# Performance work log

Hardware: AMD Instinct MI355X
Metric: run time of the kernel (lower is better)

Reference implementation:

```python
import jax, jax.numpy as jnp
import numpy as np

B, L, J, CL, CJ, DM, NH, NB, OBS = 8192, 32, 31, 4, 8, 64, 4, 3, 128
TOK = CL * 16  # 64, flattened per-link token size
HD = DM // NH


def _ln(x, g, b):
    m = x.mean(-1, keepdims=True)
    v = ((x - m) ** 2).mean(-1, keepdims=True)
    return (x - m) / jnp.sqrt(v + 1e-5) * g + b


def setup_inputs() -> dict:
    key = jax.random.key(0)
    ks = list(jax.random.split(key, 30))
    rn = lambda k, s, sc=0.05: jax.random.normal(k, s, dtype=jnp.float32) * sc
    inp = {
        'obs': jax.random.normal(ks[0], (B, OBS), dtype=jnp.float32),
        # per-link MLP encoders (obs->64->TOK), stacked over links
        'link_enc_w1': rn(ks[1], (L, 64, OBS)),
        'link_enc_b1': jnp.zeros((L, 64), jnp.float32),
        'link_enc_w2': rn(ks[2], (L, TOK, 64)),
        'link_enc_b2': jnp.zeros((L, TOK), jnp.float32),
        # per-joint encoders (obs->CJ)
        'joint_enc_w': rn(ks[3], (J, CJ, OBS)),
        'joint_enc_b': jnp.zeros((J, CJ), jnp.float32),
        # Rodrigues kernels per block per joint
        'rod_mix': rn(ks[4], (NB, J, CL, CL), 0.2),
        'rod_theta_w': rn(ks[5], (NB, J, CL, CJ), 0.2),
        'rod_theta_b': jnp.zeros((NB, J, CL), jnp.float32),
        'rod_gen': rn(ks[6], (NB, J, 4, 4), 0.2),
        'rod_ln_g': jnp.ones((NB, L, TOK), jnp.float32),
        'rod_ln_b': jnp.zeros((NB, L, TOK), jnp.float32),
        # JointLayer linears per block per joint (TOK->CJ)
        'jl_w': rn(ks[7], (NB, J, CJ, TOK)),
        'jl_b': jnp.zeros((NB, J, CJ), jnp.float32),
        # attention per block
        'proj_in_w': rn(ks[8], (NB, DM, TOK)),
        'proj_in_b': jnp.zeros((NB, DM), jnp.float32),
        'qkv_w': rn(ks[9], (NB, 3 * DM, DM)),
        'qkv_b': jnp.zeros((NB, 3 * DM), jnp.float32),
        'attn_out_w': rn(ks[10], (NB, DM, DM)),
        'attn_out_b': jnp.zeros((NB, DM), jnp.float32),
        'proj_out_w': rn(ks[11], (NB, TOK, DM)),
        'proj_out_b': jnp.zeros((NB, TOK), jnp.float32),
        'attn_ln_g': jnp.ones((NB, TOK), jnp.float32),
        'attn_ln_b': jnp.zeros((NB, TOK), jnp.float32),
        # kinematic chain edges: parent j -> child j+1
        'p_idx': jnp.arange(J, dtype=jnp.int32),
        'c_idx': jnp.arange(1, J + 1, dtype=jnp.int32),
    }
    return inp


def _forward(obs, link_enc_w1, link_enc_b1, link_enc_w2, link_enc_b2,
             joint_enc_w, joint_enc_b, rod_mix, rod_theta_w, rod_theta_b,
             rod_gen, rod_ln_g, rod_ln_b, jl_w, jl_b, proj_in_w, proj_in_b,
             qkv_w, qkv_b, attn_out_w, attn_out_b, proj_out_w, proj_out_b,
             attn_ln_g, attn_ln_b, p_idx, c_idx):
    b = obs.shape[0]
    # ---- encode ----
    h = jax.nn.elu(jnp.einsum('bo,lho->blh', obs, link_enc_w1) + link_enc_b1)
    link = jnp.einsum('blh,lgh->blg', h, link_enc_w2) + link_enc_b2  # (B,L,TOK)
    link = link.reshape(b, L, CL, 4, 4)
    joint = jnp.einsum('bo,jco->bjc', obs, joint_enc_w) + joint_enc_b  # (B,J,CJ)
    for t in range(NB):
        # ---- RodriguesLayer (reads input link feats; unique children -> parallel) ----
        Fp = link[:, p_idx]  # (B,J,CL,4,4)
        Fc = link[:, c_idx]
        Fm = jnp.einsum('joc,bjcxy->bjoxy', rod_mix[t], Fp)
        a = jnp.einsum('bjc,joc->bjo', joint, rod_theta_w[t]) + rod_theta_b[t]  # (B,J,CL)
        G = rod_gen[t]
        GF = jnp.einsum('jxy,bjoyz->bjoxz', G, Fm)
        GGF = jnp.einsum('jxy,bjoyz->bjoxz', G, GF)
        s = jnp.sin(a)[..., None, None]
        c1 = (1.0 - jnp.cos(a))[..., None, None]
        Ft = Fm + s * GF + c1 * GGF  # Rodrigues: F + sin(a) G F + (1-cos(a)) G^2 F
        comb = _ln((Fc + Ft).reshape(b, J, TOK), rod_ln_g[t][c_idx], rod_ln_b[t][c_idx])
        root = _ln(link[:, 0].reshape(b, TOK), rod_ln_g[t][0], rod_ln_b[t][0])
        link = link.at[:, 0].set(root.reshape(b, CL, 4, 4))
        link = link.at[:, c_idx].set(comb.reshape(b, J, CL, 4, 4))
        # ---- JointLayer ----
        child_flat = link[:, c_idx].reshape(b, J, TOK)
        joint = jnp.einsum('bjh,jch->bjc', child_flat, jl_w[t]) + jl_b[t] + joint
        # ---- SelfAttentionLayer ----
        tok = link.reshape(b, L, TOK)
        x = jnp.einsum('blh,dh->bld', tok, proj_in_w[t]) + proj_in_b[t]
        qkv = jnp.einsum('bld,ed->ble', x, qkv_w[t]) + qkv_b[t]
        q, k, v = jnp.split(qkv, 3, axis=-1)
        hsplit = lambda z: z.reshape(b, L, NH, HD).transpose(0, 2, 1, 3)
        q, k, v = hsplit(q), hsplit(k), hsplit(v)
        attn = jax.nn.softmax(jnp.einsum('bhqd,bhkd->bhqk', q, k) / jnp.sqrt(jnp.float32(HD)), axis=-1)
        o = jnp.einsum('bhqk,bhkd->bhqd', attn, v).transpose(0, 2, 1, 3).reshape(b, L, DM)
        o = jnp.einsum('bld,ed->ble', o, attn_out_w[t]) + attn_out_b[t]
        o = jnp.einsum('bld,hd->blh', o, proj_out_w[t]) + proj_out_b[t]
        tok = _ln(tok + o, attn_ln_g[t], attn_ln_b[t])
        link = tok.reshape(b, L, CL, 4, 4)
    return jnp.concatenate([link.reshape(b, -1), joint.reshape(b, -1)], axis=-1)


def reference(obs, link_enc_w1, link_enc_b1, link_enc_w2, link_enc_b2,
              joint_enc_w, joint_enc_b, rod_mix, rod_theta_w, rod_theta_b,
              rod_gen, rod_ln_g, rod_ln_b, jl_w, jl_b, proj_in_w, proj_in_b,
              qkv_w, qkv_b, attn_out_w, attn_out_b, proj_out_w, proj_out_b,
              attn_ln_g, attn_ln_b, p_idx, c_idx):
    return _forward(obs, link_enc_w1, link_enc_b1, link_enc_w2, link_enc_b2,
                    joint_enc_w, joint_enc_b, rod_mix, rod_theta_w, rod_theta_b,
                    rod_gen, rod_ln_g, rod_ln_b, jl_w, jl_b, proj_in_w, proj_in_b,
                    qkv_w, qkv_b, attn_out_w, attn_out_b, proj_out_w, proj_out_b,
                    attn_ln_g, attn_ln_b, p_idx, c_idx)
```

## Files before the change

### kernel.cpp

```cpp
#include <hip/hip_runtime.h>

typedef unsigned short u16;
typedef __attribute__((ext_vector_type(8))) short bh8;
typedef __attribute__((ext_vector_type(4))) float fx4;

__device__ __forceinline__ u16 f2b(float f){
  unsigned int u = __float_as_uint(f);
  u += 0x7fffu + ((u>>16)&1u);
  return (u16)(u>>16);
}
__device__ __forceinline__ float b2f(u16 h){
  return __uint_as_float(((unsigned int)h)<<16);
}
__device__ __forceinline__ bh8 ldf(const u16* p){
  return *(const bh8*)p;
}
#define MFMA(a,b,c) __builtin_amdgcn_mfma_f32_16x16x32_bf16((a),(b),(c),0,0,0)

static const long OFF_W1 = 0;
static const long OFF_W2 = 278528;
static const long OFF_WJ = 425984;
static const long OFF_PI = 460800;
static const long OFF_QK = 474624;
static const long OFF_AO = 516096;
static const long OFF_PO = 529920;
static const long OFF_QP = 543744;
static const long OFF_OP = 585216;
static const long OFF_BQ = 599040;
static const long OFF_BO = 600192;
static const long WS_U16 = 600576;

__global__ __launch_bounds__(256) void conv_kernel(
  const float* __restrict__ w1, const float* __restrict__ w2,
  const float* __restrict__ wj,
  const float* __restrict__ pi, const float* __restrict__ pib,
  const float* __restrict__ qk, const float* __restrict__ qkb,
  const float* __restrict__ ao, const float* __restrict__ aob,
  const float* __restrict__ po, const float* __restrict__ pob,
  u16* __restrict__ ws)
{
  const int stride = gridDim.x*blockDim.x;
  const int g0 = blockIdx.x*blockDim.x + threadIdx.x;
  for (int i=g0;i<2048*136;i+=stride){ int r=i/136,c=i-r*136; ws[OFF_W1+i]= (c<128)? f2b(w1[(long)r*128+c]) : (u16)0; }
  for (int i=g0;i<2048*72;i+=stride){ int r=i/72,c=i-r*72; ws[OFF_W2+i]= (c<64)? f2b(w2[(long)(r<<6)+c]) : (u16)0; }
  for (int i=g0;i<256*136;i+=stride){ int r=i/136,c=i-r*136; ws[OFF_WJ+i]= (c<128&&r<248)? f2b(wj[(long)(r<<7)+c]) : (u16)0; }
  for (int i=g0;i<192*72;i+=stride){ int r=i/72,c=i-r*72; ws[OFF_PI+i]= (c<64)? f2b(pi[(r<<6)+c]) : (u16)0; }
  for (int i=g0;i<576*72;i+=stride){ int r=i/72,c=i-r*72; ws[OFF_QK+i]= (c<64)? f2b(qk[(r<<6)+c]) : (u16)0; }
  for (int i=g0;i<192*72;i+=stride){ int r=i/72,c=i-r*72; ws[OFF_AO+i]= (c<64)? f2b(ao[(r<<6)+c]) : (u16)0; }
  for (int i=g0;i<192*72;i+=stride){ int r=i/72,c=i-r*72; ws[OFF_PO+i]= (c<64)? f2b(po[(r<<6)+c]) : (u16)0; }

  for (int i=g0;i<3*192*64;i+=stride){
    int t=i/(192*64), rem=i-t*192*64, e=rem>>6, h=rem&63;
    const float* qw = qk + ((long)t*192+e)*64;
    const float* pw = pi + (long)t*4096 + h;
    float acc=0.f;
    #pragma unroll 8
    for (int d=0;d<64;d++) acc += qw[d]*pw[d*64];
    ws[OFF_QP + (long)t*13824 + e*72 + h] = f2b(acc);
  }
  for (int i=g0;i<3*192;i+=stride){
    int t=i/192, e=i-t*192;
    const float* qw = qk + ((long)t*192+e)*64;
    const float* pb = pib + (long)t*64;
    float acc = qkb[(long)t*192+e];
    #pragma unroll 8
    for (int d=0;d<64;d++) acc += qw[d]*pb[d];
    ((float*)(ws+OFF_BQ))[i] = acc;
  }
  for (int i=g0;i<3*64*64;i+=stride){
    int t=i/(64*64), rem=i-t*64*64, n=rem>>6, d=rem&63;
    const float* pw = po + (long)t*4096 + (long)n*64;
    const float* aw = ao + (long)t*4096 + d;
    float acc=0.f;
    #pragma unroll 8
    for (int e=0;e<64;e++) acc += pw[e]*aw[e*64];
    ws[OFF_OP + (long)t*4608 + n*72 + d] = f2b(acc);
  }
  for (int i=g0;i<3*64;i+=stride){
    int t=i/64, n=i-t*64;
    const float* pw = po + (long)t*4096 + (long)n*64;
    const float* ab = aob + (long)t*64;
    float acc = pob[(long)t*64+n];
    #pragma unroll 8
    for (int e=0;e<64;e++) acc += pw[e]*ab[e];
    ((float*)(ws+OFF_BO))[i] = acc;
  }
}

struct __align__(16) SMem1 {
  u16 obs_l[16][136];
  u16 wa[64][136];
  u16 wb[64][72];
  u16 hb[16][72];
};

template<bool PRE>
__global__ __launch_bounds__(256) void enc_kernel(
  const float* __restrict__ obs, const float* __restrict__ w1,
  const float* __restrict__ b1, const float* __restrict__ w2,
  const float* __restrict__ b2, const float* __restrict__ wj,
  const float* __restrict__ bj, const u16* __restrict__ wsw,
  float* __restrict__ dout)
{
  __shared__ SMem1 s;
  const int tid = threadIdx.x;
  const int wave = tid>>6, lane = tid&63;
  const int g = lane>>4, cc = lane&15;
  const long bb = (long)blockIdx.x*16;

  for (int i=tid;i<16*128;i+=256){ int r=i>>7,c=i&127; s.obs_l[r][c]=f2b(obs[(bb+r)*128+c]); }

  for (int l=0;l<32;l++){
    if (PRE){
      const u16* s1 = wsw + OFF_W1 + (long)l*8704;
      for (int i=tid*8;i<8704;i+=2048) *(bh8*)(&s.wa[0][0]+i) = *(const bh8*)(s1+i);
      const u16* s2 = wsw + OFF_W2 + (long)l*4608;
      for (int i=tid*8;i<4608;i+=2048) *(bh8*)(&s.wb[0][0]+i) = *(const bh8*)(s2+i);
    } else {
      for (int i=tid;i<64*128;i+=256){ s.wa[i>>7][i&127]=f2b(w1[(long)l*8192+i]); }
      for (int i=tid;i<64*64;i+=256){ s.wb[i>>6][i&63]=f2b(w2[(long)l*4096+i]); }
    }
    __syncthreads();
    {
      fx4 acc = {0.f,0.f,0.f,0.f};
      #pragma unroll
      for (int ks=0;ks<4;ks++)
        acc = MFMA(ldf(&s.obs_l[cc][ks*32+g*8]), ldf(&s.wa[wave*16+cc][ks*32+g*8]), acc);
      int col = wave*16+cc;
      float bias = b1[l*64+col];
      #pragma unroll
      for (int r=0;r<4;r++){
        float v = acc[r]+bias;
        v = v>0.f ? v : expm1f(v);
        s.hb[g*4+r][col] = f2b(v);
      }
    }
    __syncthreads();
    {
      fx4 acc = {0.f,0.f,0.f,0.f};
      #pragma unroll
      for (int ks=0;ks<2;ks++)
        acc = MFMA(ldf(&s.hb[cc][ks*32+g*8]), ldf(&s.wb[wave*16+cc][ks*32+g*8]), acc);
      int col = wave*16+cc;
      float bias = b2[l*64+col];
      #pragma unroll
      for (int r=0;r<4;r++)
        dout[(bb+g*4+r)*2296 + l*64 + col] = acc[r]+bias;
    }
    __syncthreads();
  }
  for (int ci=0;ci<4;ci++){
    if (PRE){
      const u16* sj = wsw + OFF_WJ + (long)ci*8704;
      for (int i=tid*8;i<8704;i+=2048) *(bh8*)(&s.wa[0][0]+i) = *(const bh8*)(sj+i);
    } else {
      for (int i=tid;i<64*128;i+=256){
        int r=i>>7,c=i&127; int grow=ci*64+r;
        s.wa[r][c] = (grow<248)? f2b(wj[(long)grow*128+c]) : (u16)0;
      }
    }
    __syncthreads();
    fx4 acc={0.f,0.f,0.f,0.f};
    #pragma unroll
    for (int ks=0;ks<4;ks++)
      acc = MFMA(ldf(&s.obs_l[cc][ks*32+g*8]), ldf(&s.wa[wave*16+cc][ks*32+g*8]), acc);
    int ncol = ci*64 + wave*16 + cc;
    if (ncol<248){
      float bias = bj[ncol];
      #pragma unroll
      for (int r=0;r<4;r++)
        dout[(bb+g*4+r)*2296 + 2048 + ncol] = acc[r]+bias;
    }
    __syncthreads();
  }
}

struct __align__(16) SMem2 {
  float tokf[4][32][68];
  u16   tokb[4][32][72];
  u16   xs[4*32*72];
  u16   qs[4*32*72];
  u16   kk[4*32*72];
  u16   vT[4][64][40];
  float joint[4][31][8];
  union {
    u16 w[192*72];
    u16 p[8][32][40];
  } u;
};
static_assert(sizeof(SMem2) <= 163840, "LDS overflow");

template<int NT, class EPI>
__device__ __forceinline__ void gemm8(const u16* A, const u16* W,
                                      int wave, int lane, EPI epi){
  const int g = lane>>4, cc = lane&15;
  const int row = wave*16 + cc;
  bh8 a0 = ldf(&A[row*72 + g*8]);
  bh8 a1 = ldf(&A[row*72 + 32 + g*8]);
  #pragma unroll
  for (int nt=0;nt<NT;nt++){
    bh8 b0 = ldf(&W[(nt*16+cc)*72 + g*8]);
    bh8 b1 = ldf(&W[(nt*16+cc)*72 + 32 + g*8]);
    fx4 acc = {0.f,0.f,0.f,0.f};
    acc = MFMA(a0,b0,acc);
    acc = MFMA(a1,b1,acc);
    epi(nt, wave, acc);
  }
}

template<bool PRE>
__device__ __forceinline__ void stageW(u16* dst, const u16* wsrc, const float* fsrc, int rows){
  if (PRE){
    const int n = rows*72;
    for (int i=threadIdx.x*8; i<n; i+=4096)
      *(bh8*)(dst+i) = *(const bh8*)(wsrc+i);
  } else {
    const int n = rows*64;
    for (int i=threadIdx.x; i<n; i+=512)
      dst[(i>>6)*72 + (i&63)] = f2b(fsrc[i]);
  }
}

__device__ __forceinline__ void rodrigues_phase(SMem2& s, int t, int tid,
  const float* __restrict__ rod_mix, const float* __restrict__ rod_theta_w,
  const float* __restrict__ rod_theta_b, const float* __restrict__ rod_gen,
  const float* __restrict__ rod_ln_g, const float* __restrict__ rod_ln_b)
{
  const int unit = tid>>2, o = tid&3;
  const int b = unit>>5, row = unit&31;
  float nv[16];
  if (row == 0){
    #pragma unroll
    for (int i=0;i<16;i++) nv[i] = s.tokf[b][0][o*16+i];
  } else {
    const int j = row-1;
    const long wj = (long)t*31 + j;
    const float* mixp = rod_mix + wj*16 + o*4;
    const float* thwp = rod_theta_w + wj*32 + o*8;
    const float* genp = rod_gen + wj*16;
    float a = rod_theta_b[wj*4+o];
    #pragma unroll
    for (int c8=0;c8<8;c8++) a += s.joint[b][j][c8]*thwp[c8];
    float sn = sinf(a), c1 = 1.f - cosf(a);
    const float m0 = mixp[0], m1 = mixp[1], m2 = mixp[2], m3 = mixp[3];
    float G[16];
    #pragma unroll
    for (int e=0;e<16;e++) G[e] = genp[e];
    #pragma unroll
    for (int z=0;z<4;z++){
      float fm[4], gf[4], gg[4];
      #pragma unroll
      for (int x=0;x<4;x++)
        fm[x] = m0*s.tokf[b][j][     x*4+z] + m1*s.tokf[b][j][16 + x*4+z]
              + m2*s.tokf[b][j][32 + x*4+z] + m3*s.tokf[b][j][48 + x*4+z];
      #pragma unroll
      for (int x=0;x<4;x++)
        gf[x] = G[x*4+0]*fm[0] + G[x*4+1]*fm[1] + G[x*4+2]*fm[2] + G[x*4+3]*fm[3];
      #pragma unroll
      for (int x=0;x<4;x++)
        gg[x] = G[x*4+0]*gf[0] + G[x*4+1]*gf[1] + G[x*4+2]*gf[2] + G[x*4+3]*gf[3];
      #pragma unroll
      for (int x=0;x<4;x++)
        nv[x*4+z] = fm[x] + sn*gf[x] + c1*gg[x] + s.tokf[b][row][o*16+x*4+z];
    }
  }
  float sum=0.f, ssq=0.f;
  #pragma unroll
  for (int i=0;i<16;i++){ sum+=nv[i]; ssq+=nv[i]*nv[i]; }
  sum += __shfl_xor(sum,1); ssq += __shfl_xor(ssq,1);
  sum += __shfl_xor(sum,2); ssq += __shfl_xor(ssq,2);
  float mean = sum*(1.f/64.f);
  float var  = ssq*(1.f/64.f) - mean*mean;
  float rstd = rsqrtf(var + 1e-5f);
  const float* lng = rod_ln_g + ((long)t*32+row)*64 + o*16;
  const float* lnb = rod_ln_b + ((long)t*32+row)*64 + o*16;
  #pragma unroll
  for (int i=0;i<16;i++)
    nv[i] = (nv[i]-mean)*rstd*lng[i] + lnb[i];
  __syncthreads();
  #pragma unroll
  for (int i=0;i<16;i++){
    s.tokf[b][row][o*16+i] = nv[i];
    s.tokb[b][row][o*16+i] = f2b(nv[i]);
  }
}

__device__ __forceinline__ void attn_phase(SMem2& s, int wave, int g, int cc){
  const int b = wave>>1;
  const u16* qb = s.qs + b*32*72;
  const u16* kb = s.kk + b*32*72;
  u16* ob = s.xs + b*32*72;
  bh8 z8 = {0,0,0,0,0,0,0,0};
  #pragma unroll
  for (int hh=0;hh<2;hh++){
    const int h = (wave&1) + 2*hh;
    bh8 qf[2], kf[2];
    #pragma unroll
    for (int it=0;it<2;it++)
      qf[it] = (g<2) ? ldf(&qb[(it*16+cc)*72 + h*16 + g*8]) : z8;
    #pragma unroll
    for (int jt=0;jt<2;jt++)
      kf[jt] = (g<2) ? ldf(&kb[(jt*16+cc)*72 + h*16 + g*8]) : z8;
    fx4 sacc[2][2];
    #pragma unroll
    for (int it=0;it<2;it++)
      #pragma unroll
      for (int jt=0;jt<2;jt++){
        fx4 z = {0.f,0.f,0.f,0.f};
        sacc[it][jt] = MFMA(qf[it], kf[jt], z);
      }
    float pn[2][2][4];
    #pragma unroll
    for (int it=0;it<2;it++)
      #pragma unroll
      for (int r=0;r<4;r++){
        float v0 = sacc[it][0][r], v1 = sacc[it][1][r];
        float m = fmaxf(v0,v1);
        #pragma unroll
        for (int msk=1; msk<16; msk<<=1) m = fmaxf(m, __shfl_xor(m,msk));
        float e0 = __expf((v0-m)*0.25f);
        float e1 = __expf((v1-m)*0.25f);
        float sm = e0+e1;
        #pragma unroll
        for (int msk=1; msk<16; msk<<=1) sm += __shfl_xor(sm,msk);
        float inv = 1.f/sm;
        pn[it][0][r]=e0*inv; pn[it][1][r]=e1*inv;
      }
    #pragma unroll
    for (int it=0;it<2;it++)
      #pragma unroll
      for (int jt=0;jt<2;jt++)
        #pragma unroll
        for (int r=0;r<4;r++)
          s.u.p[wave][it*16+g*4+r][jt*16+cc] = f2b(pn[it][jt][r]);
    bh8 vf = ldf(&s.vT[b][h*16+cc][g*8]);
    #pragma unroll
    for (int it=0;it<2;it++){
      bh8 pf = ldf(&s.u.p[wave][it*16+cc][g*8]);
      fx4 z = {0.f,0.f,0.f,0.f};
      fx4 oacc = MFMA(pf, vf, z);
      #pragma unroll
      for (int r=0;r<4;r++)
        ob[(it*16+g*4+r)*72 + h*16+cc] = f2b(oacc[r]);
    }
  }
}

__device__ __forceinline__ void attnln_phase(SMem2& s, int t, int tid,
  const float* __restrict__ attn_ln_g, const float* __restrict__ attn_ln_b)
{
  const int unit = tid>>2, o = tid&3;
  const int b = unit>>5, row = unit&31;
  float v[16];
  #pragma unroll
  for (int i=0;i<16;i++) v[i] = s.tokf[b][row][o*16+i];
  float sum=0.f, ssq=0.f;
  #pragma unroll
  for (int i=0;i<16;i++){ sum+=v[i]; ssq+=v[i]*v[i]; }
  sum += __shfl_xor(sum,1); ssq += __shfl_xor(ssq,1);
  sum += __shfl_xor(sum,2); ssq += __shfl_xor(ssq,2);
  float mean = sum*(1.f/64.f);
  float var  = ssq*(1.f/64.f) - mean*mean;
  float rstd = rsqrtf(var + 1e-5f);
  const float* lg = attn_ln_g + (long)t*64 + o*16;
  const float* lb = attn_ln_b + (long)t*64 + o*16;
  #pragma unroll
  for (int i=0;i<16;i++){
    float ov = (v[i]-mean)*rstd*lg[i] + lb[i];
    s.tokf[b][row][o*16+i] = ov;
    s.tokb[b][row][o*16+i] = f2b(ov);
  }
}

__global__ __launch_bounds__(512,1) void rodri_fold(
  const float* __restrict__ rod_mix, const float* __restrict__ rod_theta_w,
  const float* __restrict__ rod_theta_b, const float* __restrict__ rod_gen,
  const float* __restrict__ rod_ln_g, const float* __restrict__ rod_ln_b,
  const float* __restrict__ jl_w, const float* __restrict__ jl_b,
  const float* __restrict__ attn_ln_g, const float* __restrict__ attn_ln_b,
  const u16* __restrict__ wsw, float* __restrict__ dout)
{
  __shared__ SMem2 s;
  const int tid = threadIdx.x;
  const int wave = tid>>6, lane = tid&63;
  const int g = lane>>4, cc = lane&15;
  const long bb = (long)blockIdx.x*4;

  for (int i=tid;i<4*2048;i+=512){
    int b=i>>11, r=i&2047;
    float v = dout[(bb+b)*2296 + r];
    s.tokf[b][r>>6][r&63] = v;
    s.tokb[b][r>>6][r&63] = f2b(v);
  }
  for (int i=tid;i<4*248;i+=512){
    int b=i/248, r=i-b*248;
    s.joint[b][r>>3][r&7] = dout[(bb+b)*2296 + 2048 + r];
  }
  __syncthreads();

  for (int t=0;t<3;t++){
    rodrigues_phase(s, t, tid, rod_mix, rod_theta_w, rod_theta_b, rod_gen, rod_ln_g, rod_ln_b);
    __syncthreads();

    if (tid < 248){
      int j = tid>>3, c8 = tid&7;
      const float* wrow = jl_w + (((long)t*31 + j)*8 + c8)*64;
      float bias = jl_b[((long)t*31+j)*8 + c8];
      float a0=0.f,a1=0.f,a2=0.f,a3=0.f;
      for (int h=0;h<64;h++){
        float w = wrow[h];
        a0 += w*b2f(s.tokb[0][j+1][h]);
        a1 += w*b2f(s.tokb[1][j+1][h]);
        a2 += w*b2f(s.tokb[2][j+1][h]);
        a3 += w*b2f(s.tokb[3][j+1][h]);
      }
      s.joint[0][j][c8] += a0 + bias;
      s.joint[1][j][c8] += a1 + bias;
      s.joint[2][j][c8] += a2 + bias;
      s.joint[3][j][c8] += a3 + bias;
    }
    __syncthreads();

    stageW<true>(s.u.w, wsw+OFF_QP+(long)t*13824, nullptr, 192);
    __syncthreads();
    {
      const float* bq = (const float*)(wsw + OFF_BQ) + (long)t*192;
      gemm8<12>(&s.tokb[0][0][0], s.u.w, wave, lane,
        [&](int nt,int mtile,const fx4& acc){
          int col = nt*16+cc;
          float bias = bq[col];
          #pragma unroll
          for (int r=0;r<4;r++){
            int rg = mtile*16+g*4+r;
            float v = acc[r]+bias;
            int b = rg>>5, l = rg&31;
            if (col<64)       s.qs[rg*72+col]      = f2b(v);
            else if (col<128) s.kk[rg*72+(col-64)] = f2b(v);
            else              s.vT[b][col-128][l]  = f2b(v);
          }
        });
    }
    __syncthreads();

    attn_phase(s, wave, g, cc);
    __syncthreads();

    stageW<true>(s.u.w, wsw+OFF_OP+(long)t*4608, nullptr, 64);
    __syncthreads();
    {
      const float* bo = (const float*)(wsw + OFF_BO) + (long)t*64;
      gemm8<4>(s.xs, s.u.w, wave, lane,
        [&](int nt,int mtile,const fx4& acc){
          int col = nt*16+cc;
          float bias = bo[col];
          #pragma unroll
          for (int r=0;r<4;r++){
            int rg = mtile*16+g*4+r;
            int b = rg>>5, l = rg&31;
            s.tokf[b][l][col] += acc[r] + bias;
          }
        });
    }
    __syncthreads();

    attnln_phase(s, t, tid, attn_ln_g, attn_ln_b);
    __syncthreads();
  }

  for (int i=tid;i<4*2048;i+=512){
    int b=i>>11, r=i&2047;
    dout[(bb+b)*2296 + r] = s.tokf[b][r>>6][r&63];
  }
  for (int i=tid;i<4*248;i+=512){
    int b=i/248, r=i-b*248;
    dout[(bb+b)*2296 + 2048 + r] = s.joint[b][r>>3][r&7];
  }
}

__global__ __launch_bounds__(512,1) void rodri_nopre(
  const float* __restrict__ rod_mix, const float* __restrict__ rod_theta_w,
  const float* __restrict__ rod_theta_b, const float* __restrict__ rod_gen,
  const float* __restrict__ rod_ln_g, const float* __restrict__ rod_ln_b,
  const float* __restrict__ jl_w, const float* __restrict__ jl_b,
  const float* __restrict__ proj_in_w, const float* __restrict__ proj_in_b,
  const float* __restrict__ qkv_w, const float* __restrict__ qkv_b,
  const float* __restrict__ attn_out_w, const float* __restrict__ attn_out_b,
  const float* __restrict__ proj_out_w, const float* __restrict__ proj_out_b,
  const float* __restrict__ attn_ln_g, const float* __restrict__ attn_ln_b,
  float* __restrict__ dout)
{
  __shared__ SMem2 s;
  const int tid = threadIdx.x;
  const int wave = tid>>6, lane = tid&63;
  const int g = lane>>4, cc = lane&15;
  const long bb = (long)blockIdx.x*4;

  for (int i=tid;i<4*2048;i+=512){
    int b=i>>11, r=i&2047;
    float v = dout[(bb+b)*2296 + r];
    s.tokf[b][r>>6][r&63] = v;
    s.tokb[b][r>>6][r&63] = f2b(v);
  }
  for (int i=tid;i<4*248;i+=512){
    int b=i/248, r=i-b*248;
    s.joint[b][r>>3][r&7] = dout[(bb+b)*2296 + 2048 + r];
  }
  __syncthreads();

  for (int t=0;t<3;t++){
    rodrigues_phase(s, t, tid, rod_mix, rod_theta_w, rod_theta_b, rod_gen, rod_ln_g, rod_ln_b);
    __syncthreads();

    if (tid < 248){
      int j = tid>>3, c8 = tid&7;
      const float* wrow = jl_w + (((long)t*31 + j)*8 + c8)*64;
      float bias = jl_b[((long)t*31+j)*8 + c8];
      float a0=0.f,a1=0.f,a2=0.f,a3=0.f;
      for (int h=0;h<64;h++){
        float w = wrow[h];
        a0 += w*b2f(s.tokb[0][j+1][h]);
        a1 += w*b2f(s.tokb[1][j+1][h]);
        a2 += w*b2f(s.tokb[2][j+1][h]);
        a3 += w*b2f(s.tokb[3][j+1][h]);
      }
      s.joint[0][j][c8] += a0 + bias;
      s.joint[1][j][c8] += a1 + bias;
      s.joint[2][j][c8] += a2 + bias;
      s.joint[3][j][c8] += a3 + bias;
    }
    __syncthreads();

    stageW<false>(s.u.w, nullptr, proj_in_w+(long)t*4096, 64);
    __syncthreads();
    {
      const float* bp = proj_in_b + (long)t*64;
      gemm8<4>(&s.tokb[0][0][0], s.u.w, wave, lane,
        [&](int nt,int mtile,const fx4& acc){
          int col = nt*16+cc;
          float bias = bp[col];
          #pragma unroll
          for (int r=0;r<4;r++){
            int rg = mtile*16+g*4+r;
            s.xs[rg*72+col] = f2b(acc[r]+bias);
          }
        });
    }
    __syncthreads();

    stageW<false>(s.u.w, nullptr, qkv_w+(long)t*12288, 192);
    __syncthreads();
    {
      const float* bq = qkv_b + (long)t*192;
      gemm8<12>(s.xs, s.u.w, wave, lane,
        [&](int nt,int mtile,const fx4& acc){
          int col = nt*16+cc;
          float bias = bq[col];
          #pragma unroll
          for (int r=0;r<4;r++){
            int rg = mtile*16+g*4+r;
            float v = acc[r]+bias;
            int b = rg>>5, l = rg&31;
            if (col<64)       s.qs[rg*72+col]      = f2b(v);
            else if (col<128) s.kk[rg*72+(col-64)] = f2b(v);
            else              s.vT[b][col-128][l]  = f2b(v);
          }
        });
    }
    __syncthreads();

    attn_phase(s, wave, g, cc);
    __syncthreads();

    stageW<false>(s.u.w, nullptr, attn_out_w+(long)t*4096, 64);
    __syncthreads();
    {
      const float* bo = attn_out_b + (long)t*64;
      gemm8<4>(s.xs, s.u.w, wave, lane,
        [&](int nt,int mtile,const fx4& acc){
          int col = nt*16+cc;
          float bias = bo[col];
          #pragma unroll
          for (int r=0;r<4;r++){
            int rg = mtile*16+g*4+r;
            s.qs[rg*72+col] = f2b(acc[r]+bias);
          }
        });
    }
    __syncthreads();

    stageW<false>(s.u.w, nullptr, proj_out_w+(long)t*4096, 64);
    __syncthreads();
    {
      const float* bp2 = proj_out_b + (long)t*64;
      gemm8<4>(s.qs, s.u.w, wave, lane,
        [&](int nt,int mtile,const fx4& acc){
          int col = nt*16+cc;
          float bias = bp2[col];
          #pragma unroll
          for (int r=0;r<4;r++){
            int rg = mtile*16+g*4+r;
            int b = rg>>5, l = rg&31;
            s.tokf[b][l][col] += acc[r] + bias;
          }
        });
    }
    __syncthreads();

    attnln_phase(s, t, tid, attn_ln_g, attn_ln_b);
    __syncthreads();
  }

  for (int i=tid;i<4*2048;i+=512){
    int b=i>>11, r=i&2047;
    dout[(bb+b)*2296 + r] = s.tokf[b][r>>6][r&63];
  }
  for (int i=tid;i<4*248;i+=512){
    int b=i/248, r=i-b*248;
    dout[(bb+b)*2296 + 2048 + r] = s.joint[b][r>>3][r&7];
  }
}

extern "C" void kernel_launch(void* const* d_in, const int* in_sizes, int n_in,
                              void* d_out, int out_size, void* d_ws, size_t ws_size,
                              hipStream_t stream) {
  (void)in_sizes; (void)n_in; (void)out_size;
  float* out = (float*)d_out;
  u16* ws = (u16*)d_ws;
  const bool pre = (ws_size >= (size_t)WS_U16*2);

  if (pre){
    conv_kernel<<<dim3(512), dim3(256), 0, stream>>>(
      (const float*)d_in[1], (const float*)d_in[3], (const float*)d_in[5],
      (const float*)d_in[15], (const float*)d_in[16],
      (const float*)d_in[17], (const float*)d_in[18],
      (const float*)d_in[19], (const float*)d_in[20],
      (const float*)d_in[21], (const float*)d_in[22], ws);
    enc_kernel<true><<<dim3(512), dim3(256), 0, stream>>>(
      (const float*)d_in[0], (const float*)d_in[1], (const float*)d_in[2],
      (const float*)d_in[3], (const float*)d_in[4], (const float*)d_in[5],
      (const float*)d_in[6], ws, out);
    rodri_fold<<<dim3(2048), dim3(512), 0, stream>>>(
      (const float*)d_in[7],  (const float*)d_in[8],  (const float*)d_in[9],
      (const float*)d_in[10], (const float*)d_in[11], (const float*)d_in[12],
      (const float*)d_in[13], (const float*)d_in[14],
      (const float*)d_in[23], (const float*)d_in[24],
      ws, out);
  } else {
    enc_kernel<false><<<dim3(512), dim3(256), 0, stream>>>(
      (const float*)d_in[0], (const float*)d_in[1], (const float*)d_in[2],
      (const float*)d_in[3], (const float*)d_in[4], (const float*)d_in[5],
      (const float*)d_in[6], ws, out);
    rodri_nopre<<<dim3(2048), dim3(512), 0, stream>>>(
      (const float*)d_in[7],  (const float*)d_in[8],  (const float*)d_in[9],
      (const float*)d_in[10], (const float*)d_in[11], (const float*)d_in[12],
      (const float*)d_in[13], (const float*)d_in[14], (const float*)d_in[15],
      (const float*)d_in[16], (const float*)d_in[17], (const float*)d_in[18],
      (const float*)d_in[19], (const float*)d_in[20], (const float*)d_in[21],
      (const float*)d_in[22], (const float*)d_in[23], (const float*)d_in[24],
      out);
  }
}
```

Before: 485.6 us.

## Run rodri_fold with 1024 threads and prestage all per-step weights together

The fused Rodrigues/attention kernel now launches 16 waves per block instead of 8. The folded proj_in+qkv weights and the folded out-projection weights are loaded into LDS together, overlapping with the joint-layer update, which removes one stage/sync pair per step. The GEMMs split N-tiles across wave pairs, and attention gives each wave a single (batch, head). Elementwise phases use only half the threads, and LDS grows with a separate wop buffer and larger P scratch, while the block still runs one per CU.

```diff
diff --git a/kernel.cpp b/kernel.cpp
--- a/kernel.cpp
+++ b/kernel.cpp
@@ -175,6 +175,289 @@
   }
 }
 
+struct __align__(16) SMemF {
+  float tokf[4][32][66];
+  u16   tokb[4][32][72];
+  u16   qs[4*32*72];
+  u16   kk[4*32*72];
+  u16   vT[4][64][40];
+  float joint[4][31][8];
+  u16   wop[64*72];
+  union {
+    u16 w[192*72];
+    u16 p[16][32][40];
+  } u;
+};
+static_assert(sizeof(SMemF) <= 163840, "LDS overflow");
+static_assert(sizeof(SMemF) > 81920, "must stay 1 block/CU (co-residency corrupts: R2/3/9/11/12)");
+
+__global__ __launch_bounds__(1024,1) void rodri_fold(
+  const float* __restrict__ rod_mix, const float* __restrict__ rod_theta_w,
+  const float* __restrict__ rod_theta_b, const float* __restrict__ rod_gen,
+  const float* __restrict__ rod_ln_g, const float* __restrict__ rod_ln_b,
+  const float* __restrict__ jl_w, const float* __restrict__ jl_b,
+  const float* __restrict__ attn_ln_g, const float* __restrict__ attn_ln_b,
+  const u16* __restrict__ wsw, float* __restrict__ dout)
+{
+  __shared__ SMemF s;
+  const int tid = threadIdx.x;
+  const int wave = tid>>6, lane = tid&63;
+  const int g = lane>>4, cc = lane&15;
+  const long bb = (long)blockIdx.x*4;
+
+  for (int i=tid;i<4*2048;i+=1024){
+    int b=i>>11, r=i&2047;
+    float v = dout[(bb+b)*2296 + r];
+    s.tokf[b][r>>6][r&63] = v;
+    s.tokb[b][r>>6][r&63] = f2b(v);
+  }
+  for (int i=tid;i<4*248;i+=1024){
+    int b=i/248, r=i-b*248;
+    s.joint[b][r>>3][r&7] = dout[(bb+b)*2296 + 2048 + r];
+  }
+  __syncthreads();
+
+  for (int t=0;t<3;t++){
+    {
+      const bool active = (tid < 512);
+      const int unit = tid>>2, o = tid&3;
+      const int b = (unit>>5)&3, row = unit&31;
+      float nv[16];
+      if (active){
+        if (row == 0){
+          #pragma unroll
+          for (int i=0;i<16;i++) nv[i] = s.tokf[b][0][o*16+i];
+        } else {
+          const int j = row-1;
+          const long wj = (long)t*31 + j;
+          const float* mixp = rod_mix + wj*16 + o*4;
+          const float* thwp = rod_theta_w + wj*32 + o*8;
+          const float* genp = rod_gen + wj*16;
+          float a = rod_theta_b[wj*4+o];
+          #pragma unroll
+          for (int c8=0;c8<8;c8++) a += s.joint[b][j][c8]*thwp[c8];
+          float sn = sinf(a), c1 = 1.f - cosf(a);
+          const float m0 = mixp[0], m1 = mixp[1], m2 = mixp[2], m3 = mixp[3];
+          float G[16];
+          #pragma unroll
+          for (int e=0;e<16;e++) G[e] = genp[e];
+          #pragma unroll
+          for (int z=0;z<4;z++){
+            float fm[4], gf[4], gg[4];
+            #pragma unroll
+            for (int x=0;x<4;x++)
+              fm[x] = m0*s.tokf[b][j][     x*4+z] + m1*s.tokf[b][j][16 + x*4+z]
+                    + m2*s.tokf[b][j][32 + x*4+z] + m3*s.tokf[b][j][48 + x*4+z];
+            #pragma unroll
+            for (int x=0;x<4;x++)
+              gf[x] = G[x*4+0]*fm[0] + G[x*4+1]*fm[1] + G[x*4+2]*fm[2] + G[x*4+3]*fm[3];
+            #pragma unroll
+            for (int x=0;x<4;x++)
+              gg[x] = G[x*4+0]*gf[0] + G[x*4+1]*gf[1] + G[x*4+2]*gf[2] + G[x*4+3]*gf[3];
+            #pragma unroll
+            for (int x=0;x<4;x++)
+              nv[x*4+z] = fm[x] + sn*gf[x] + c1*gg[x] + s.tokf[b][row][o*16+x*4+z];
+          }
+        }
+        float sum=0.f, ssq=0.f;
+        #pragma unroll
+        for (int i=0;i<16;i++){ sum+=nv[i]; ssq+=nv[i]*nv[i]; }
+        sum += __shfl_xor(sum,1); ssq += __shfl_xor(ssq,1);
+        sum += __shfl_xor(sum,2); ssq += __shfl_xor(ssq,2);
+        float mean = sum*(1.f/64.f);
+        float var  = ssq*(1.f/64.f) - mean*mean;
+        float rstd = rsqrtf(var + 1e-5f);
+        const float* lng = rod_ln_g + ((long)t*32+row)*64 + o*16;
+        const float* lnb = rod_ln_b + ((long)t*32+row)*64 + o*16;
+        #pragma unroll
+        for (int i=0;i<16;i++)
+          nv[i] = (nv[i]-mean)*rstd*lng[i] + lnb[i];
+      }
+      __syncthreads();
+      if (active){
+        #pragma unroll
+        for (int i=0;i<16;i++){
+          s.tokf[b][row][o*16+i] = nv[i];
+          s.tokb[b][row][o*16+i] = f2b(nv[i]);
+        }
+      }
+    }
+    __syncthreads();
+
+    for (int i=tid*8;i<13824;i+=8192)
+      *(bh8*)(s.u.w+i) = *(const bh8*)(wsw+OFF_QP+(long)t*13824+i);
+    for (int i=tid*8;i<4608;i+=8192)
+      *(bh8*)(s.wop+i) = *(const bh8*)(wsw+OFF_OP+(long)t*4608+i);
+    if (tid < 248){
+      int j = tid>>3, c8 = tid&7;
+      const float* wrow = jl_w + (((long)t*31 + j)*8 + c8)*64;
+      float bias = jl_b[((long)t*31+j)*8 + c8];
+      float a0=0.f,a1=0.f,a2=0.f,a3=0.f;
+      for (int h=0;h<64;h++){
+        float w = wrow[h];
+        a0 += w*b2f(s.tokb[0][j+1][h]);
+        a1 += w*b2f(s.tokb[1][j+1][h]);
+        a2 += w*b2f(s.tokb[2][j+1][h]);
+        a3 += w*b2f(s.tokb[3][j+1][h]);
+      }
+      s.joint[0][j][c8] += a0 + bias;
+      s.joint[1][j][c8] += a1 + bias;
+      s.joint[2][j][c8] += a2 + bias;
+      s.joint[3][j][c8] += a3 + bias;
+    }
+    __syncthreads();
+
+    {
+      const float* bq = (const float*)(wsw + OFF_BQ) + (long)t*192;
+      const int mtile = wave>>1, half = wave&1;
+      const int row = mtile*16 + cc;
+      const u16* A = &s.tokb[0][0][0];
+      bh8 a0 = ldf(&A[row*72 + g*8]);
+      bh8 a1 = ldf(&A[row*72 + 32 + g*8]);
+      #pragma unroll
+      for (int k6=0;k6<6;k6++){
+        int nt = half + 2*k6;
+        bh8 b0 = ldf(&s.u.w[(nt*16+cc)*72 + g*8]);
+        bh8 b1 = ldf(&s.u.w[(nt*16+cc)*72 + 32 + g*8]);
+        fx4 acc = {0.f,0.f,0.f,0.f};
+        acc = MFMA(a0,b0,acc);
+        acc = MFMA(a1,b1,acc);
+        int col = nt*16+cc;
+        float bias = bq[col];
+        #pragma unroll
+        for (int r=0;r<4;r++){
+          int rg = mtile*16+g*4+r;
+          float v = acc[r]+bias;
+          int b = rg>>5, l = rg&31;
+          if (col<64)       s.qs[rg*72+col]      = f2b(v);
+          else if (col<128) s.kk[rg*72+(col-64)] = f2b(v);
+          else              s.vT[b][col-128][l]  = f2b(v);
+        }
+      }
+    }
+    __syncthreads();
+
+    {
+      const int b = wave>>2, h = wave&3;
+      const u16* qb = s.qs + b*2304;
+      u16* kb = s.kk + b*2304;
+      bh8 z8 = {0,0,0,0,0,0,0,0};
+      bh8 qf[2], kf[2];
+      #pragma unroll
+      for (int it=0;it<2;it++)
+        qf[it] = (g<2) ? ldf(&qb[(it*16+cc)*72 + h*16 + g*8]) : z8;
+      #pragma unroll
+      for (int jt=0;jt<2;jt++)
+        kf[jt] = (g<2) ? ldf(&kb[(jt*16+cc)*72 + h*16 + g*8]) : z8;
+      fx4 sacc[2][2];
+      #pragma unroll
+      for (int it=0;it<2;it++)
+        #pragma unroll
+        for (int jt=0;jt<2;jt++){
+          fx4 z = {0.f,0.f,0.f,0.f};
+          sacc[it][jt] = MFMA(qf[it], kf[jt], z);
+        }
+      float pn[2][2][4];
+      #pragma unroll
+      for (int it=0;it<2;it++)
+        #pragma unroll
+        for (int r=0;r<4;r++){
+          float v0 = sacc[it][0][r], v1 = sacc[it][1][r];
+          float m = fmaxf(v0,v1);
+          #pragma unroll
+          for (int msk=1; msk<16; msk<<=1) m = fmaxf(m, __shfl_xor(m,msk));
+          float e0 = __expf((v0-m)*0.25f);
+          float e1 = __expf((v1-m)*0.25f);
+          float sm = e0+e1;
+          #pragma unroll
+          for (int msk=1; msk<16; msk<<=1) sm += __shfl_xor(sm,msk);
+          float inv = 1.f/sm;
+          pn[it][0][r]=e0*inv; pn[it][1][r]=e1*inv;
+        }
+      #pragma unroll
+      for (int it=0;it<2;it++)
+        #pragma unroll
+        for (int jt=0;jt<2;jt++)
+          #pragma unroll
+          for (int r=0;r<4;r++)
+            s.u.p[wave][it*16+g*4+r][jt*16+cc] = f2b(pn[it][jt][r]);
+      bh8 vf = ldf(&s.vT[b][h*16+cc][g*8]);
+      #pragma unroll
+      for (int it=0;it<2;it++){
+        bh8 pf = ldf(&s.u.p[wave][it*16+cc][g*8]);
+        fx4 z = {0.f,0.f,0.f,0.f};
+        fx4 oacc = MFMA(pf, vf, z);
+        #pragma unroll
+        for (int r=0;r<4;r++)
+          kb[(it*16+g*4+r)*72 + h*16+cc] = f2b(oacc[r]);
+      }
+    }
+    __syncthreads();
+
+    {
+      const float* bo = (const float*)(wsw + OFF_BO) + (long)t*64;
+      const int mtile = wave>>1, half = wave&1;
+      const int row = mtile*16 + cc;
+      bh8 a0 = ldf(&s.kk[row*72 + g*8]);
+      bh8 a1 = ldf(&s.kk[row*72 + 32 + g*8]);
+      #pragma unroll
+      for (int k2=0;k2<2;k2++){
+        int nt = half + 2*k2;
+        bh8 b0 = ldf(&s.wop[(nt*16+cc)*72 + g*8]);
+        bh8 b1 = ldf(&s.wop[(nt*16+cc)*72 + 32 + g*8]);
+        fx4 acc = {0.f,0.f,0.f,0.f};
+        acc = MFMA(a0,b0,acc);
+        acc = MFMA(a1,b1,acc);
+        int col = nt*16+cc;
+        float bias = bo[col];
+        #pragma unroll
+        for (int r=0;r<4;r++){
+          int rg = mtile*16+g*4+r;
+          s.tokf[rg>>5][rg&31][col] += acc[r] + bias;
+        }
+      }
+    }
+    __syncthreads();
+
+    {
+      const bool active = (tid < 512);
+      const int unit = tid>>2, o = tid&3;
+      const int b = (unit>>5)&3, row = unit&31;
+      if (active){
+        float v[16];
+        #pragma unroll
+        for (int i=0;i<16;i++) v[i] = s.tokf[b][row][o*16+i];
+        float sum=0.f, ssq=0.f;
+        #pragma unroll
+        for (int i=0;i<16;i++){ sum+=v[i]; ssq+=v[i]*v[i]; }
+        sum += __shfl_xor(sum,1); ssq += __shfl_xor(ssq,1);
+        sum += __shfl_xor(sum,2); ssq += __shfl_xor(ssq,2);
+        float mean = sum*(1.f/64.f);
+        float var  = ssq*(1.f/64.f) - mean*mean;
+        float rstd = rsqrtf(var + 1e-5f);
+        const float* lg = attn_ln_g + (long)t*64 + o*16;
+        const float* lb = attn_ln_b + (long)t*64 + o*16;
+        #pragma unroll
+        for (int i=0;i<16;i++){
+          float ov = (v[i]-mean)*rstd*lg[i] + lb[i];
+          s.tokf[b][row][o*16+i] = ov;
+          s.tokb[b][row][o*16+i] = f2b(ov);
+        }
+      }
+    }
+    __syncthreads();
+  }
+
+  for (int i=tid;i<4*2048;i+=1024){
+    int b=i>>11, r=i&2047;
+    dout[(bb+b)*2296 + r] = s.tokf[b][r>>6][r&63];
+  }
+  for (int i=tid;i<4*248;i+=1024){
+    int b=i/248, r=i-b*248;
+    dout[(bb+b)*2296 + 2048 + r] = s.joint[b][r>>3][r&7];
+  }
+}
+
 struct __align__(16) SMem2 {
   float tokf[4][32][68];
   u16   tokb[4][32][72];
@@ -208,273 +491,10 @@
   }
 }
 
-template<bool PRE>
-__device__ __forceinline__ void stageW(u16* dst, const u16* wsrc, const float* fsrc, int rows){
-  if (PRE){
-    const int n = rows*72;
-    for (int i=threadIdx.x*8; i<n; i+=4096)
-      *(bh8*)(dst+i) = *(const bh8*)(wsrc+i);
-  } else {
-    const int n = rows*64;
-    for (int i=threadIdx.x; i<n; i+=512)
-      dst[(i>>6)*72 + (i&63)] = f2b(fsrc[i]);
-  }
-}
-
-__device__ __forceinline__ void rodrigues_phase(SMem2& s, int t, int tid,
-  const float* __restrict__ rod_mix, const float* __restrict__ rod_theta_w,
-  const float* __restrict__ rod_theta_b, const float* __restrict__ rod_gen,
-  const float* __restrict__ rod_ln_g, const float* __restrict__ rod_ln_b)
-{
-  const int unit = tid>>2, o = tid&3;
-  const int b = unit>>5, row = unit&31;
-  float nv[16];
-  if (row == 0){
-    #pragma unroll
-    for (int i=0;i<16;i++) nv[i] = s.tokf[b][0][o*16+i];
-  } else {
-    const int j = row-1;
-    const long wj = (long)t*31 + j;
-    const float* mixp = rod_mix + wj*16 + o*4;
-    const float* thwp = rod_theta_w + wj*32 + o*8;
-    const float* genp = rod_gen + wj*16;
-    float a = rod_theta_b[wj*4+o];
-    #pragma unroll
-    for (int c8=0;c8<8;c8++) a += s.joint[b][j][c8]*thwp[c8];
-    float sn = sinf(a), c1 = 1.f - cosf(a);
-    const float m0 = mixp[0], m1 = mixp[1], m2 = mixp[2], m3 = mixp[3];
-    float G[16];
-    #pragma unroll
-    for (int e=0;e<16;e++) G[e] = genp[e];
-    #pragma unroll
-    for (int z=0;z<4;z++){
-      float fm[4], gf[4], gg[4];
-      #pragma unroll
-      for (int x=0;x<4;x++)
-        fm[x] = m0*s.tokf[b][j][     x*4+z] + m1*s.tokf[b][j][16 + x*4+z]
-              + m2*s.tokf[b][j][32 + x*4+z] + m3*s.tokf[b][j][48 + x*4+z];
-      #pragma unroll
-      for (int x=0;x<4;x++)
-        gf[x] = G[x*4+0]*fm[0] + G[x*4+1]*fm[1] + G[x*4+2]*fm[2] + G[x*4+3]*fm[3];
-      #pragma unroll
-      for (int x=0;x<4;x++)
-        gg[x] = G[x*4+0]*gf[0] + G[x*4+1]*gf[1] + G[x*4+2]*gf[2] + G[x*4+3]*gf[3];
-      #pragma unroll
-      for (int x=0;x<4;x++)
-        nv[x*4+z] = fm[x] + sn*gf[x] + c1*gg[x] + s.tokf[b][row][o*16+x*4+z];
-    }
-  }
-  float sum=0.f, ssq=0.f;
-  #pragma unroll
-  for (int i=0;i<16;i++){ sum+=nv[i]; ssq+=nv[i]*nv[i]; }
-  sum += __shfl_xor(sum,1); ssq += __shfl_xor(ssq,1);
-  sum += __shfl_xor(sum,2); ssq += __shfl_xor(ssq,2);
-  float mean = sum*(1.f/64.f);
-  float var  = ssq*(1.f/64.f) - mean*mean;
-  float rstd = rsqrtf(var + 1e-5f);
-  const float* lng = rod_ln_g + ((long)t*32+row)*64 + o*16;
-  const float* lnb = rod_ln_b + ((long)t*32+row)*64 + o*16;
-  #pragma unroll
-  for (int i=0;i<16;i++)
-    nv[i] = (nv[i]-mean)*rstd*lng[i] + lnb[i];
-  __syncthreads();
-  #pragma unroll
-  for (int i=0;i<16;i++){
-    s.tokf[b][row][o*16+i] = nv[i];
-    s.tokb[b][row][o*16+i] = f2b(nv[i]);
-  }
-}
-
-__device__ __forceinline__ void attn_phase(SMem2& s, int wave, int g, int cc){
-  const int b = wave>>1;
-  const u16* qb = s.qs + b*32*72;
-  const u16* kb = s.kk + b*32*72;
-  u16* ob = s.xs + b*32*72;
-  bh8 z8 = {0,0,0,0,0,0,0,0};
-  #pragma unroll
-  for (int hh=0;hh<2;hh++){
-    const int h = (wave&1) + 2*hh;
-    bh8 qf[2], kf[2];
-    #pragma unroll
-    for (int it=0;it<2;it++)
-      qf[it] = (g<2) ? ldf(&qb[(it*16+cc)*72 + h*16 + g*8]) : z8;
-    #pragma unroll
-    for (int jt=0;jt<2;jt++)
-      kf[jt] = (g<2) ? ldf(&kb[(jt*16+cc)*72 + h*16 + g*8]) : z8;
-    fx4 sacc[2][2];
-    #pragma unroll
-    for (int it=0;it<2;it++)
-      #pragma unroll
-      for (int jt=0;jt<2;jt++){
-        fx4 z = {0.f,0.f,0.f,0.f};
-        sacc[it][jt] = MFMA(qf[it], kf[jt], z);
-      }
-    float pn[2][2][4];
-    #pragma unroll
-    for (int it=0;it<2;it++)
-      #pragma unroll
-      for (int r=0;r<4;r++){
-        float v0 = sacc[it][0][r], v1 = sacc[it][1][r];
-        float m = fmaxf(v0,v1);
-        #pragma unroll
-        for (int msk=1; msk<16; msk<<=1) m = fmaxf(m, __shfl_xor(m,msk));
-        float e0 = __expf((v0-m)*0.25f);
-        float e1 = __expf((v1-m)*0.25f);
-        float sm = e0+e1;
-        #pragma unroll
-        for (int msk=1; msk<16; msk<<=1) sm += __shfl_xor(sm,msk);
-        float inv = 1.f/sm;
-        pn[it][0][r]=e0*inv; pn[it][1][r]=e1*inv;
-      }
-    #pragma unroll
-    for (int it=0;it<2;it++)
-      #pragma unroll
-      for (int jt=0;jt<2;jt++)
-        #pragma unroll
-        for (int r=0;r<4;r++)
-          s.u.p[wave][it*16+g*4+r][jt*16+cc] = f2b(pn[it][jt][r]);
-    bh8 vf = ldf(&s.vT[b][h*16+cc][g*8]);
-    #pragma unroll
-    for (int it=0;it<2;it++){
-      bh8 pf = ldf(&s.u.p[wave][it*16+cc][g*8]);
-      fx4 z = {0.f,0.f,0.f,0.f};
-      fx4 oacc = MFMA(pf, vf, z);
-      #pragma unroll
-      for (int r=0;r<4;r++)
-        ob[(it*16+g*4+r)*72 + h*16+cc] = f2b(oacc[r]);
-    }
-  }
-}
-
-__device__ __forceinline__ void attnln_phase(SMem2& s, int t, int tid,
-  const float* __restrict__ attn_ln_g, const float* __restrict__ attn_ln_b)
-{
-  const int unit = tid>>2, o = tid&3;
-  const int b = unit>>5, row = unit&31;
-  float v[16];
-  #pragma unroll
-  for (int i=0;i<16;i++) v[i] = s.tokf[b][row][o*16+i];
-  float sum=0.f, ssq=0.f;
-  #pragma unroll
-  for (int i=0;i<16;i++){ sum+=v[i]; ssq+=v[i]*v[i]; }
-  sum += __shfl_xor(sum,1); ssq += __shfl_xor(ssq,1);
-  sum += __shfl_xor(sum,2); ssq += __shfl_xor(ssq,2);
-  float mean = sum*(1.f/64.f);
-  float var  = ssq*(1.f/64.f) - mean*mean;
-  float rstd = rsqrtf(var + 1e-5f);
-  const float* lg = attn_ln_g + (long)t*64 + o*16;
-  const float* lb = attn_ln_b + (long)t*64 + o*16;
-  #pragma unroll
-  for (int i=0;i<16;i++){
-    float ov = (v[i]-mean)*rstd*lg[i] + lb[i];
-    s.tokf[b][row][o*16+i] = ov;
-    s.tokb[b][row][o*16+i] = f2b(ov);
-  }
-}
-
-__global__ __launch_bounds__(512,1) void rodri_fold(
-  const float* __restrict__ rod_mix, const float* __restrict__ rod_theta_w,
-  const float* __restrict__ rod_theta_b, const float* __restrict__ rod_gen,
-  const float* __restrict__ rod_ln_g, const float* __restrict__ rod_ln_b,
-  const float* __restrict__ jl_w, const float* __restrict__ jl_b,
-  const float* __restrict__ attn_ln_g, const float* __restrict__ attn_ln_b,
-  const u16* __restrict__ wsw, float* __restrict__ dout)
-{
-  __shared__ SMem2 s;
-  const int tid = threadIdx.x;
-  const int wave = tid>>6, lane = tid&63;
-  const int g = lane>>4, cc = lane&15;
-  const long bb = (long)blockIdx.x*4;
-
-  for (int i=tid;i<4*2048;i+=512){
-    int b=i>>11, r=i&2047;
-    float v = dout[(bb+b)*2296 + r];
-    s.tokf[b][r>>6][r&63] = v;
-    s.tokb[b][r>>6][r&63] = f2b(v);
-  }
-  for (int i=tid;i<4*248;i+=512){
-    int b=i/248, r=i-b*248;
-    s.joint[b][r>>3][r&7] = dout[(bb+b)*2296 + 2048 + r];
-  }
-  __syncthreads();
-
-  for (int t=0;t<3;t++){
-    rodrigues_phase(s, t, tid, rod_mix, rod_theta_w, rod_theta_b, rod_gen, rod_ln_g, rod_ln_b);
-    __syncthreads();
-
-    if (tid < 248){
-      int j = tid>>3, c8 = tid&7;
-      const float* wrow = jl_w + (((long)t*31 + j)*8 + c8)*64;
-      float bias = jl_b[((long)t*31+j)*8 + c8];
-      float a0=0.f,a1=0.f,a2=0.f,a3=0.f;
-      for (int h=0;h<64;h++){
-        float w = wrow[h];
-        a0 += w*b2f(s.tokb[0][j+1][h]);
-        a1 += w*b2f(s.tokb[1][j+1][h]);
-        a2 += w*b2f(s.tokb[2][j+1][h]);
-        a3 += w*b2f(s.tokb[3][j+1][h]);
-      }
-      s.joint[0][j][c8] += a0 + bias;
-      s.joint[1][j][c8] += a1 + bias;
-      s.joint[2][j][c8] += a2 + bias;
-      s.joint[3][j][c8] += a3 + bias;
-    }
-    __syncthreads();
-
-    stageW<true>(s.u.w, wsw+OFF_QP+(long)t*13824, nullptr, 192);
-    __syncthreads();
-    {
-      const float* bq = (const float*)(wsw + OFF_BQ) + (long)t*192;
-      gemm8<12>(&s.tokb[0][0][0], s.u.w, wave, lane,
-        [&](int nt,int mtile,const fx4& acc){
-          int col = nt*16+cc;
-          float bias = bq[col];
-          #pragma unroll
-          for (int r=0;r<4;r++){
-            int rg = mtile*16+g*4+r;
-            float v = acc[r]+bias;
-            int b = rg>>5, l = rg&31;
-            if (col<64)       s.qs[rg*72+col]      = f2b(v);
-            else if (col<128) s.kk[rg*72+(col-64)] = f2b(v);
-            else              s.vT[b][col-128][l]  = f2b(v);
-          }
-        });
-    }
-    __syncthreads();
-
-    attn_phase(s, wave, g, cc);
-    __syncthreads();
-
-    stageW<true>(s.u.w, wsw+OFF_OP+(long)t*4608, nullptr, 64);
-    __syncthreads();
-    {
-      const float* bo = (const float*)(wsw + OFF_BO) + (long)t*64;
-      gemm8<4>(s.xs, s.u.w, wave, lane,
-        [&](int nt,int mtile,const fx4& acc){
-          int col = nt*16+cc;
-          float bias = bo[col];
-          #pragma unroll
-          for (int r=0;r<4;r++){
-            int rg = mtile*16+g*4+r;
-            int b = rg>>5, l = rg&31;
-            s.tokf[b][l][col] += acc[r] + bias;
-          }
-        });
-    }
-    __syncthreads();
-
-    attnln_phase(s, t, tid, attn_ln_g, attn_ln_b);
-    __syncthreads();
-  }
-
-  for (int i=tid;i<4*2048;i+=512){
-    int b=i>>11, r=i&2047;
-    dout[(bb+b)*2296 + r] = s.tokf[b][r>>6][r&63];
-  }
-  for (int i=tid;i<4*248;i+=512){
-    int b=i/248, r=i-b*248;
-    dout[(bb+b)*2296 + 2048 + r] = s.joint[b][r>>3][r&7];
-  }
+__device__ __forceinline__ void stageWF(u16* dst, const float* fsrc, int rows){
+  const int n = rows*64;
+  for (int i=threadIdx.x; i<n; i+=512)
+    dst[(i>>6)*72 + (i&63)] = f2b(fsrc[i]);
 }
 
 __global__ __launch_bounds__(512,1) void rodri_nopre(
@@ -508,7 +528,65 @@
   __syncthreads();
 
   for (int t=0;t<3;t++){
-    rodrigues_phase(s, t, tid, rod_mix, rod_theta_w, rod_theta_b, rod_gen, rod_ln_g, rod_ln_b);
+    {
+      const int unit = tid>>2, o = tid&3;
+      const int b = unit>>5, row = unit&31;
+      float nv[16];
+      if (row == 0){
+        #pragma unroll
+        for (int i=0;i<16;i++) nv[i] = s.tokf[b][0][o*16+i];
+      } else {
+        const int j = row-1;
+        const long wj = (long)t*31 + j;
+        const float* mixp = rod_mix + wj*16 + o*4;
+        const float* thwp = rod_theta_w + wj*32 + o*8;
+        const float* genp = rod_gen + wj*16;
+        float a = rod_theta_b[wj*4+o];
+        #pragma unroll
+        for (int c8=0;c8<8;c8++) a += s.joint[b][j][c8]*thwp[c8];
+        float sn = sinf(a), c1 = 1.f - cosf(a);
+        const float m0 = mixp[0], m1 = mixp[1], m2 = mixp[2], m3 = mixp[3];
+        float G[16];
+        #pragma unroll
+        for (int e=0;e<16;e++) G[e] = genp[e];
+        #pragma unroll
+        for (int z=0;z<4;z++){
+          float fm[4], gf[4], gg[4];
+          #pragma unroll
+          for (int x=0;x<4;x++)
+            fm[x] = m0*s.tokf[b][j][     x*4+z] + m1*s.tokf[b][j][16 + x*4+z]
+                  + m2*s.tokf[b][j][32 + x*4+z] + m3*s.tokf[b][j][48 + x*4+z];
+          #pragma unroll
+          for (int x=0;x<4;x++)
+            gf[x] = G[x*4+0]*fm[0] + G[x*4+1]*fm[1] + G[x*4+2]*fm[2] + G[x*4+3]*fm[3];
+          #pragma unroll
+          for (int x=0;x<4;x++)
+            gg[x] = G[x*4+0]*gf[0] + G[x*4+1]*gf[1] + G[x*4+2]*gf[2] + G[x*4+3]*gf[3];
+          #pragma unroll
+          for (int x=0;x<4;x++)
+            nv[x*4+z] = fm[x] + sn*gf[x] + c1*gg[x] + s.tokf[b][row][o*16+x*4+z];
+        }
+      }
+      float sum=0.f, ssq=0.f;
+      #pragma unroll
+      for (int i=0;i<16;i++){ sum+=nv[i]; ssq+=nv[i]*nv[i]; }
+      sum += __shfl_xor(sum,1); ssq += __shfl_xor(ssq,1);
+      sum += __shfl_xor(sum,2); ssq += __shfl_xor(ssq,2);
+      float mean = sum*(1.f/64.f);
+      float var  = ssq*(1.f/64.f) - mean*mean;
+      float rstd = rsqrtf(var + 1e-5f);
+      const float* lng = rod_ln_g + ((long)t*32+row)*64 + o*16;
+      const float* lnb = rod_ln_b + ((long)t*32+row)*64 + o*16;
+      #pragma unroll
+      for (int i=0;i<16;i++)
+        nv[i] = (nv[i]-mean)*rstd*lng[i] + lnb[i];
+      __syncthreads();
+      #pragma unroll
+      for (int i=0;i<16;i++){
+        s.tokf[b][row][o*16+i] = nv[i];
+        s.tokb[b][row][o*16+i] = f2b(nv[i]);
+      }
+    }
     __syncthreads();
 
     if (tid < 248){
@@ -530,7 +608,7 @@
     }
     __syncthreads();
 
-    stageW<false>(s.u.w, nullptr, proj_in_w+(long)t*4096, 64);
+    stageWF(s.u.w, proj_in_w+(long)t*4096, 64);
     __syncthreads();
     {
       const float* bp = proj_in_b + (long)t*64;
@@ -547,7 +625,7 @@
     }
     __syncthreads();
 
-    stageW<false>(s.u.w, nullptr, qkv_w+(long)t*12288, 192);
+    stageWF(s.u.w, qkv_w+(long)t*12288, 192);
     __syncthreads();
     {
       const float* bq = qkv_b + (long)t*192;
@@ -568,10 +646,69 @@
     }
     __syncthreads();
 
-    attn_phase(s, wave, g, cc);
-    __syncthreads();
-
-    stageW<false>(s.u.w, nullptr, attn_out_w+(long)t*4096, 64);
+    {
+      const int b = wave>>1;
+      const u16* qb = s.qs + b*32*72;
+      const u16* kb = s.kk + b*32*72;
+      u16* ob = s.xs + b*32*72;
+      bh8 z8 = {0,0,0,0,0,0,0,0};
+      #pragma unroll
+      for (int hh=0;hh<2;hh++){
+        const int h = (wave&1) + 2*hh;
+        bh8 qf[2], kf[2];
+        #pragma unroll
+        for (int it=0;it<2;it++)
+          qf[it] = (g<2) ? ldf(&qb[(it*16+cc)*72 + h*16 + g*8]) : z8;
+        #pragma unroll
+        for (int jt=0;jt<2;jt++)
+          kf[jt] = (g<2) ? ldf(&kb[(jt*16+cc)*72 + h*16 + g*8]) : z8;
+        fx4 sacc[2][2];
+        #pragma unroll
+        for (int it=0;it<2;it++)
+          #pragma unroll
+          for (int jt=0;jt<2;jt++){
+            fx4 z = {0.f,0.f,0.f,0.f};
+            sacc[it][jt] = MFMA(qf[it], kf[jt], z);
+          }
+        float pn[2][2][4];
+        #pragma unroll
+        for (int it=0;it<2;it++)
+          #pragma unroll
+          for (int r=0;r<4;r++){
+            float v0 = sacc[it][0][r], v1 = sacc[it][1][r];
+            float m = fmaxf(v0,v1);
+            #pragma unroll
+            for (int msk=1; msk<16; msk<<=1) m = fmaxf(m, __shfl_xor(m,msk));
+            float e0 = __expf((v0-m)*0.25f);
+            float e1 = __expf((v1-m)*0.25f);
+            float sm = e0+e1;
+            #pragma unroll
+            for (int msk=1; msk<16; msk<<=1) sm += __shfl_xor(sm,msk);
+            float inv = 1.f/sm;
+            pn[it][0][r]=e0*inv; pn[it][1][r]=e1*inv;
+          }
+        #pragma unroll
+        for (int it=0;it<2;it++)
+          #pragma unroll
+          for (int jt=0;jt<2;jt++)
+            #pragma unroll
+            for (int r=0;r<4;r++)
+              s.u.p[wave][it*16+g*4+r][jt*16+cc] = f2b(pn[it][jt][r]);
+        bh8 vf = ldf(&s.vT[b][h*16+cc][g*8]);
+        #pragma unroll
+        for (int it=0;it<2;it++){
+          bh8 pf = ldf(&s.u.p[wave][it*16+cc][g*8]);
+          fx4 z = {0.f,0.f,0.f,0.f};
+          fx4 oacc = MFMA(pf, vf, z);
+          #pragma unroll
+          for (int r=0;r<4;r++)
+            ob[(it*16+g*4+r)*72 + h*16+cc] = f2b(oacc[r]);
+        }
+      }
+    }
+    __syncthreads();
+
+    stageWF(s.u.w, attn_out_w+(long)t*4096, 64);
     __syncthreads();
     {
       const float* bo = attn_out_b + (long)t*64;
@@ -588,7 +725,7 @@
     }
     __syncthreads();
 
-    stageW<false>(s.u.w, nullptr, proj_out_w+(long)t*4096, 64);
+    stageWF(s.u.w, proj_out_w+(long)t*4096, 64);
     __syncthreads();
     {
       const float* bp2 = proj_out_b + (long)t*64;
@@ -606,7 +743,29 @@
     }
     __syncthreads();
 
-    attnln_phase(s, t, tid, attn_ln_g, attn_ln_b);
+    {
+      const int unit = tid>>2, o = tid&3;
+      const int b = unit>>5, row = unit&31;
+      float v[16];
+      #pragma unroll
+      for (int i=0;i<16;i++) v[i] = s.tokf[b][row][o*16+i];
+      float sum=0.f, ssq=0.f;
+      #pragma unroll
+      for (int i=0;i<16;i++){ sum+=v[i]; ssq+=v[i]*v[i]; }
+      sum += __shfl_xor(sum,1); ssq += __shfl_xor(ssq,1);
+      sum += __shfl_xor(sum,2); ssq += __shfl_xor(ssq,2);
+      float mean = sum*(1.f/64.f);
+      float var  = ssq*(1.f/64.f) - mean*mean;
+      float rstd = rsqrtf(var + 1e-5f);
+      const float* lg = attn_ln_g + (long)t*64 + o*16;
+      const float* lb = attn_ln_b + (long)t*64 + o*16;
+      #pragma unroll
+      for (int i=0;i<16;i++){
+        float ov = (v[i]-mean)*rstd*lg[i] + lb[i];
+        s.tokf[b][row][o*16+i] = ov;
+        s.tokb[b][row][o*16+i] = f2b(ov);
+      }
+    }
     __syncthreads();
   }
 
@@ -639,7 +798,7 @@
       (const float*)d_in[0], (const float*)d_in[1], (const float*)d_in[2],
       (const float*)d_in[3], (const float*)d_in[4], (const float*)d_in[5],
       (const float*)d_in[6], ws, out);
-    rodri_fold<<<dim3(2048), dim3(512), 0, stream>>>(
+    rodri_fold<<<dim3(2048), dim3(1024), 0, stream>>>(
       (const float*)d_in[7],  (const float*)d_in[8],  (const float*)d_in[9],
       (const float*)d_in[10], (const float*)d_in[11], (const float*)d_in[12],
       (const float*)d_in[13], (const float*)d_in[14],
```

New measurement: 712.5 us. 1.47x slower.
